# Performance work log

Measured on AMD Instinct MI355X. Metric: run time of the kernel, lower is better.

## Reference

```python
import jax, jax.numpy as jnp
import numpy as np

B, N, C = 16, 1024, 768
H, HD = 9, 64  # num_active_heads, head_dim


def setup_inputs() -> dict:
    key = jax.random.key(0)
    ks = jax.random.split(key, 5)
    x = jax.random.normal(ks[0], (B, N, C), dtype=jnp.float32)
    qkv_w = jax.random.normal(ks[1], (3 * H * HD, C), dtype=jnp.float32) * (1.0 / np.sqrt(C))
    qkv_b = jax.random.normal(ks[2], (3 * H * HD,), dtype=jnp.float32) * 0.02
    proj_w = jax.random.normal(ks[3], (C, H * HD), dtype=jnp.float32) * (1.0 / np.sqrt(H * HD))
    proj_b = jax.random.normal(ks[4], (C,), dtype=jnp.float32) * 0.02
    return {"x": x, "qkv_w": qkv_w, "qkv_b": qkv_b, "proj_w": proj_w, "proj_b": proj_b}


def reference(x, qkv_w, qkv_b, proj_w, proj_b):
    b, n, c = x.shape
    # qkv projection: [B,N,3*H*HD] -> [3,B,H,N,HD]
    qkv = (x @ qkv_w.T + qkv_b).reshape(b, n, 3, H, HD).transpose(2, 0, 3, 1, 4)
    q, k, v = qkv[0], qkv[1], qkv[2]
    scale = HD ** -0.5
    attn = jnp.einsum('bhqd,bhkd->bhqk', q, k) * scale  # [B,H,N,N]
    attn = jax.nn.softmax(attn, axis=-1)
    out = jnp.einsum('bhqk,bhkd->bhqd', attn, v)  # [B,H,N,HD]
    out = out.transpose(0, 2, 1, 3).reshape(b, n, H * HD)
    return out @ proj_w.T + proj_b
```

## Files before the change

### kernel.cpp

```cpp
#include <hip/hip_runtime.h>


typedef _Float16 f16x8 __attribute__((ext_vector_type(8)));
typedef _Float16 f16x4 __attribute__((ext_vector_type(4)));
typedef __fp16   h16x2 __attribute__((ext_vector_type(2)));
typedef float    f32x4 __attribute__((ext_vector_type(4)));

#define MFMA16(a, b, c) __builtin_amdgcn_mfma_f32_16x16x32_f16(a, b, c, 0, 0, 0)

__device__ __forceinline__ void gld16(const _Float16* g, _Float16* l) {
  __builtin_amdgcn_global_load_lds((const __attribute__((address_space(1))) void*)g,
                                   (__attribute__((address_space(3))) void*)l, 16, 0, 0);
}

__global__ __launch_bounds__(256) void cvt_swz(const float* __restrict__ src,
                                               _Float16* __restrict__ dst,
                                               int rows_src, int cpr, int total) {
  const int g = blockIdx.x * 256 + threadIdx.x;
  if (g >= total) return;
  const int row = g / cpr;
  const int c = g - row * cpr;
  const int L = cpr * 8;
  const int pos = (c & ~7) | ((c ^ row) & 7);
  union { f16x8 v; h16x2 h[4]; } u;
  if (row < rows_src) {
    const float4 a = *(const float4*)(src + row * L + c * 8);
    const float4 b = *(const float4*)(src + row * L + c * 8 + 4);
    u.h[0] = __builtin_amdgcn_cvt_pkrtz(a.x, a.y);
    u.h[1] = __builtin_amdgcn_cvt_pkrtz(a.z, a.w);
    u.h[2] = __builtin_amdgcn_cvt_pkrtz(b.x, b.y);
    u.h[3] = __builtin_amdgcn_cvt_pkrtz(b.z, b.w);
  } else {
    u.v = (f16x8){};
  }
  *(f16x8*)(dst + row * L + pos * 8) = u.v;
}

__global__ __launch_bounds__(256, 4) void gemm1_qkv(const _Float16* __restrict__ A,
                                                    const _Float16* __restrict__ Bw,
                                                    const float* __restrict__ bias,
                                                    _Float16* __restrict__ Qo,
                                                    _Float16* __restrict__ Ko,
                                                    _Float16* __restrict__ Vt) {
  __shared__ __align__(16) _Float16 As[128 * 64];
  __shared__ __align__(16) _Float16 Bs[128 * 64];
  const int tid = threadIdx.x;
  const int wave = tid >> 6, lane = tid & 63;
  const int lo = lane & 15, hi = lane >> 4;
  const int wm = (wave >> 1) * 64, wn = (wave & 1) * 64;
  const int g = blockIdx.x;
  const int xcd = g & 7, i = g >> 3;
  const int mt = i / 14, ntl = i - mt * 14;
  const int m0 = (xcd * 16 + mt) * 128, n0 = ntl * 128;
  f32x4 acc[4][4] = {};
  for (int k0 = 0; k0 < 768; k0 += 64) {
    __syncthreads();
    #pragma unroll
    for (int j = 0; j < 4; ++j) {
      const int seg = wave * 4 + j;
      const int gr = seg * 8 + (lane >> 3), gc = (lane & 7) << 3;
      gld16(A + (m0 + gr) * 768 + k0 + gc, As + seg * 512);
      gld16(Bw + (n0 + gr) * 768 + k0 + gc, Bs + seg * 512);
    }
    __syncthreads();
    #pragma unroll
    for (int ks = 0; ks < 2; ++ks) {
      f16x8 af[4], bf[4];
      const int p = ((ks * 4 + hi) ^ (lo & 7)) << 3;
      #pragma unroll
      for (int t = 0; t < 4; ++t) {
        af[t] = *(const f16x8*)(As + (wm + t * 16 + lo) * 64 + p);
        bf[t] = *(const f16x8*)(Bs + (wn + t * 16 + lo) * 64 + p);
      }
      #pragma unroll
      for (int mt2 = 0; mt2 < 4; ++mt2)
        #pragma unroll
        for (int nt = 0; nt < 4; ++nt)
          acc[mt2][nt] = MFMA16(af[mt2], bf[nt], acc[mt2][nt]);
    }
  }
  const int b = m0 >> 10;
  const int nrbase = (m0 & 1023) + wm;
  #pragma unroll
  for (int nt = 0; nt < 4; ++nt) {
    const int n = n0 + wn + nt * 16 + lo;
    if (n < 1728) {
      const float bv = bias[n];
      const int t3 = n / 576;
      const int rem = n - t3 * 576;
      const int hh = rem >> 6, d = rem & 63;
      const int bh16 = (b * 9 + hh) << 16;
      if (t3 == 2) {
        _Float16* dv = Vt + bh16 + d * 1024;
        #pragma unroll
        for (int mt2 = 0; mt2 < 4; ++mt2) {
          const int nr = nrbase + mt2 * 16 + hi * 4;
          const int c = nr >> 3;
          const int pos = (c & ~7) | ((c ^ d) & 7);
          union { f16x4 v; h16x2 h[2]; } u;
          u.h[0] = __builtin_amdgcn_cvt_pkrtz(acc[mt2][nt][0] + bv, acc[mt2][nt][1] + bv);
          u.h[1] = __builtin_amdgcn_cvt_pkrtz(acc[mt2][nt][2] + bv, acc[mt2][nt][3] + bv);
          *(f16x4*)(dv + pos * 8 + (nr & 7)) = u.v;
        }
      } else if (t3 == 1) {
        _Float16* dk = Ko + bh16;
        const int ch = d >> 3, dl = d & 7;
        #pragma unroll
        for (int mt2 = 0; mt2 < 4; ++mt2) {
          const int nr = nrbase + mt2 * 16 + hi * 4;
          #pragma unroll
          for (int i2 = 0; i2 < 4; ++i2) {
            const int t = nr + i2;
            dk[t * 64 + ((ch ^ (t & 7)) << 3) + dl] = (_Float16)(acc[mt2][nt][i2] + bv);
          }
        }
      } else {
        _Float16* dq = Qo + bh16 + d;
        #pragma unroll
        for (int mt2 = 0; mt2 < 4; ++mt2) {
          const int nr = nrbase + mt2 * 16 + hi * 4;
          #pragma unroll
          for (int i2 = 0; i2 < 4; ++i2)
            dq[(nr + i2) * 64] = (_Float16)(acc[mt2][nt][i2] + bv);
        }
      }
    }
  }
}

__global__ __launch_bounds__(256, 4) void attn_fused(const _Float16* __restrict__ Qg,
                                                     const _Float16* __restrict__ Kg,
                                                     const _Float16* __restrict__ Vtg,
                                                     _Float16* __restrict__ Og) {
  __shared__ __align__(16) _Float16 Ks[2][64 * 64];
  __shared__ __align__(16) _Float16 Vts[2][64 * 64];
  __shared__ __align__(16) _Float16 Ps[4][16 * 64];
  const int tid = threadIdx.x;
  const int wave = tid >> 6, lane = tid & 63;
  const int lo = lane & 15, hi = lane >> 4;
  const int bid = blockIdx.x;
  const int xcd = bid & 7, idx = bid >> 3;
  const int bh = xcd * 18 + (idx >> 4);
  const int q0 = (idx & 15) << 6;
  const _Float16* Qp  = Qg + (bh << 16);
  const _Float16* Kp  = Kg + (bh << 16);
  const _Float16* Vtp = Vtg + (bh << 16);

  auto issue = [&](int t0, int nb) {
    #pragma unroll
    for (int j = 0; j < 2; ++j) {
      const int seg = wave * 2 + j;
      gld16(Kp + (t0 + seg * 8 + (lane >> 3)) * 64 + ((lane & 7) << 3), &Ks[nb][seg * 512]);
      gld16(Vtp + (seg * 8 + (lane >> 3)) * 1024 + t0 + ((lane & 7) << 3), &Vts[nb][seg * 512]);
    }
  };

  issue(0, 0);

  f16x8 qf[2];
  const _Float16* qrow = Qp + (q0 + wave * 16 + lo) * 64;
  qf[0] = *(const f16x8*)(qrow + hi * 8);
  qf[1] = *(const f16x8*)(qrow + (4 + hi) * 8);

  float m_run = -1e30f, l_run = 0.f;
  f32x4 accO[4] = {};
  const float cs = 0.125f * 1.44269504f;
  _Float16* Pw = Ps[wave];

  auto compute = [&](int cb) {
    const _Float16* Kc = Ks[cb];
    const _Float16* Vc = Vts[cb];
    f32x4 sacc[4] = {};
    #pragma unroll
    for (int tt = 0; tt < 4; ++tt)
      #pragma unroll
      for (int ks = 0; ks < 2; ++ks) {
        const f16x8 kf = *(const f16x8*)(Kc + (tt * 16 + lo) * 64 + (((ks * 4 + hi) ^ (lo & 7)) << 3));
        sacc[tt] = MFMA16(kf, qf[ks], sacc[tt]);
      }
    float rmax = -1e30f;
    #pragma unroll
    for (int tt = 0; tt < 4; ++tt)
      rmax = fmaxf(rmax, fmaxf(fmaxf(sacc[tt][0], sacc[tt][1]), fmaxf(sacc[tt][2], sacc[tt][3])));
    rmax = fmaxf(rmax, __shfl_xor(rmax, 16, 64));
    rmax = fmaxf(rmax, __shfl_xor(rmax, 32, 64));
    const float rs = rmax * cs;
    const bool nsk = !__all(rs <= m_run + 8.f);
    const float mnew = nsk ? fmaxf(m_run, rs) : m_run;
    const float alpha = nsk ? __builtin_amdgcn_exp2f(m_run - mnew) : 1.f;
    float rsum = 0.f;
    #pragma unroll
    for (int tt = 0; tt < 4; ++tt) {
      const float p0 = __builtin_amdgcn_exp2f(fmaf(sacc[tt][0], cs, -mnew));
      const float p1 = __builtin_amdgcn_exp2f(fmaf(sacc[tt][1], cs, -mnew));
      const float p2 = __builtin_amdgcn_exp2f(fmaf(sacc[tt][2], cs, -mnew));
      const float p3 = __builtin_amdgcn_exp2f(fmaf(sacc[tt][3], cs, -mnew));
      rsum += (p0 + p1) + (p2 + p3);
      union { f16x4 v; h16x2 h[2]; } u;
      u.h[0] = __builtin_amdgcn_cvt_pkrtz(p0, p1);
      u.h[1] = __builtin_amdgcn_cvt_pkrtz(p2, p3);
      const int c = 2 * tt + (hi >> 1);
      *(f16x4*)(Pw + lo * 64 + (((c ^ lo) & 7) << 3) + ((hi & 1) << 2)) = u.v;
    }
    rsum += __shfl_xor(rsum, 16, 64);
    rsum += __shfl_xor(rsum, 32, 64);
    l_run = l_run * alpha + rsum;
    m_run = mnew;
    if (nsk) {
      #pragma unroll
      for (int dt = 0; dt < 4; ++dt) accO[dt] *= alpha;
    }

    #pragma unroll
    for (int ks2 = 0; ks2 < 2; ++ks2) {
      const int c = 4 * ks2 + hi;
      const f16x8 pf = *(const f16x8*)(Pw + lo * 64 + (((c ^ lo) & 7) << 3));
      #pragma unroll
      for (int dt = 0; dt < 4; ++dt) {
        const int dd = dt * 16 + lo;
        const f16x8 vf = *(const f16x8*)(Vc + dd * 64 + (((c ^ dd) & 7) << 3));
        accO[dt] = MFMA16(vf, pf, accO[dt]);
      }
    }
  };

  auto step = [&](int tnext0, int cb, bool pre) {
    if (pre) {
      issue(tnext0, cb ^ 1);
      asm volatile("s_waitcnt vmcnt(4)" ::: "memory");
    } else {
      asm volatile("s_waitcnt vmcnt(0)" ::: "memory");
    }
    __builtin_amdgcn_sched_barrier(0);
    __builtin_amdgcn_s_barrier();
    compute(cb);
    __builtin_amdgcn_sched_barrier(0);
    __builtin_amdgcn_s_barrier();
  };

  #pragma unroll 1
  for (int it = 0; it < 7; ++it) {
    step((2 * it + 1) << 6, 0, true);
    step((2 * it + 2) << 6, 1, true);
  }
  step(15 << 6, 0, true);
  step(0, 1, false);

  const float inv = 1.f / l_run;
  const int b = bh / 9, hh = bh - b * 9;
  const int rq = (b << 10) + q0 + wave * 16 + lo;
  #pragma unroll
  for (int dt = 0; dt < 4; ++dt) {
    union { f16x4 v; h16x2 h[2]; } u;
    u.h[0] = __builtin_amdgcn_cvt_pkrtz(accO[dt][0] * inv, accO[dt][1] * inv);
    u.h[1] = __builtin_amdgcn_cvt_pkrtz(accO[dt][2] * inv, accO[dt][3] * inv);
    const int c = hh * 8 + dt * 2 + (hi >> 1);
    const int pos = (c & ~7) | ((c ^ rq) & 7);
    *(f16x4*)(Og + rq * 576 + pos * 8 + ((hi & 1) << 2)) = u.v;
  }
}

__global__ __launch_bounds__(256, 4) void gemm3_proj(const _Float16* __restrict__ A,
                                                     const _Float16* __restrict__ Bw,
                                                     const float* __restrict__ bias,
                                                     float* __restrict__ out) {
  __shared__ __align__(16) _Float16 As[128 * 64];
  __shared__ __align__(16) _Float16 Bs[128 * 64];
  const int tid = threadIdx.x;
  const int wave = tid >> 6, lane = tid & 63;
  const int lo = lane & 15, hi = lane >> 4;
  const int wm = (wave >> 1) * 64, wn = (wave & 1) * 64;
  const int g = blockIdx.x;
  const int xcd = g & 7, i = g >> 3;
  const int mt = i / 6, ntl = i - mt * 6;
  const int m0 = (xcd * 16 + mt) * 128, n0 = ntl * 128;
  f32x4 acc[4][4] = {};
  for (int k0 = 0; k0 < 576; k0 += 64) {
    __syncthreads();
    #pragma unroll
    for (int j = 0; j < 4; ++j) {
      const int seg = wave * 4 + j;
      const int gr = seg * 8 + (lane >> 3), gc = (lane & 7) << 3;
      gld16(A + (m0 + gr) * 576 + k0 + gc, As + seg * 512);
      gld16(Bw + (n0 + gr) * 576 + k0 + gc, Bs + seg * 512);
    }
    __syncthreads();
    #pragma unroll
    for (int ks = 0; ks < 2; ++ks) {
      f16x8 af[4], bf[4];
      const int p = ((ks * 4 + hi) ^ (lo & 7)) << 3;
      #pragma unroll
      for (int t = 0; t < 4; ++t) {
        af[t] = *(const f16x8*)(As + (wm + t * 16 + lo) * 64 + p);
        bf[t] = *(const f16x8*)(Bs + (wn + t * 16 + lo) * 64 + p);
      }
      #pragma unroll
      for (int mt2 = 0; mt2 < 4; ++mt2)
        #pragma unroll
        for (int nt = 0; nt < 4; ++nt)
          acc[mt2][nt] = MFMA16(af[mt2], bf[nt], acc[mt2][nt]);
    }
  }
  #pragma unroll
  for (int nt = 0; nt < 4; ++nt) {
    const int n = n0 + wn + nt * 16 + lo;
    const float bv = bias[n];
    #pragma unroll
    for (int mt2 = 0; mt2 < 4; ++mt2) {
      const int mrow = m0 + wm + mt2 * 16 + hi * 4;
      #pragma unroll
      for (int i2 = 0; i2 < 4; ++i2)
        out[(mrow + i2) * 768 + n] = acc[mt2][nt][i2] + bv;
    }
  }
}

extern "C" void kernel_launch(void* const* d_in, const int* in_sizes, int n_in,
                              void* d_out, int out_size, void* d_ws, size_t ws_size,
                              hipStream_t stream) {
  const float* x      = (const float*)d_in[0];
  const float* qkv_w  = (const float*)d_in[1];
  const float* qkv_b  = (const float*)d_in[2];
  const float* proj_w = (const float*)d_in[3];
  const float* proj_b = (const float*)d_in[4];
  float* out = (float*)d_out;

  char* ws = (char*)d_ws;
  _Float16* x16 = (_Float16*)(ws + 0);
  _Float16* w1p = (_Float16*)(ws + 25165824);
  _Float16* w2h = (_Float16*)(ws + 27918336);
  _Float16* Qh  = (_Float16*)(ws + 28803072);
  _Float16* Kh  = (_Float16*)(ws + 47677440);
  _Float16* Vth = (_Float16*)(ws + 66551808);
  _Float16* Oh  = (_Float16*)(ws + 85426176);

  cvt_swz<<<6144, 256, 0, stream>>>(x, x16, 16384, 96, 16384 * 96);
  cvt_swz<<<672, 256, 0, stream>>>(qkv_w, w1p, 1728, 96, 1792 * 96);
  cvt_swz<<<216, 256, 0, stream>>>(proj_w, w2h, 768, 72, 768 * 72);
  gemm1_qkv<<<1792, 256, 0, stream>>>(x16, w1p, qkv_b, Qh, Kh, Vth);
  attn_fused<<<2304, 256, 0, stream>>>(Qh, Kh, Vth, Oh);
  gemm3_proj<<<768, 256, 0, stream>>>(Oh, w2h, proj_b, out);
}
```

Before: 247.4 us.

## Single-buffer V tile in attention to raise occupancy, add MFMA priority hints

The attention kernel now keeps a single LDS buffer for the V tile instead of two. The next V tile is loaded only after the end-of-step barrier, while K stays double-buffered and is prefetched at the start of each step. This frees LDS so the launch bound can request 5 blocks per CU instead of 4. s_setprio is also raised around the MFMA sections. The cost is that each V load is exposed within a single step's QK and softmax phase rather than a full iteration, and the vmcnt accounting changes.

Measured after the change: 244.4 us. About the same (-1.2%).

```diff
diff --git a/kernel.cpp b/kernel.cpp
--- a/kernel.cpp
+++ b/kernel.cpp
@@ -128,12 +128,12 @@
   }
 }
 
-__global__ __launch_bounds__(256, 4) void attn_fused(const _Float16* __restrict__ Qg,
+__global__ __launch_bounds__(256, 5) void attn_fused(const _Float16* __restrict__ Qg,
                                                      const _Float16* __restrict__ Kg,
                                                      const _Float16* __restrict__ Vtg,
                                                      _Float16* __restrict__ Og) {
   __shared__ __align__(16) _Float16 Ks[2][64 * 64];
-  __shared__ __align__(16) _Float16 Vts[2][64 * 64];
+  __shared__ __align__(16) _Float16 Vts[64 * 64];
   __shared__ __align__(16) _Float16 Ps[4][16 * 64];
   const int tid = threadIdx.x;
   const int wave = tid >> 6, lane = tid & 63;
@@ -146,16 +146,23 @@
   const _Float16* Kp  = Kg + (bh << 16);
   const _Float16* Vtp = Vtg + (bh << 16);
 
-  auto issue = [&](int t0, int nb) {
+  auto issueK = [&](int t0, int nb) {
     #pragma unroll
     for (int j = 0; j < 2; ++j) {
       const int seg = wave * 2 + j;
       gld16(Kp + (t0 + seg * 8 + (lane >> 3)) * 64 + ((lane & 7) << 3), &Ks[nb][seg * 512]);
-      gld16(Vtp + (seg * 8 + (lane >> 3)) * 1024 + t0 + ((lane & 7) << 3), &Vts[nb][seg * 512]);
     }
   };
-
-  issue(0, 0);
+  auto issueV = [&](int t0) {
+    #pragma unroll
+    for (int j = 0; j < 2; ++j) {
+      const int seg = wave * 2 + j;
+      gld16(Vtp + (seg * 8 + (lane >> 3)) * 1024 + t0 + ((lane & 7) << 3), Vts + seg * 512);
+    }
+  };
+
+  issueK(0, 0);
+  issueV(0);
 
   f16x8 qf[2];
   const _Float16* qrow = Qp + (q0 + wave * 16 + lo) * 64;
@@ -169,8 +176,8 @@
 
   auto compute = [&](int cb) {
     const _Float16* Kc = Ks[cb];
-    const _Float16* Vc = Vts[cb];
     f32x4 sacc[4] = {};
+    __builtin_amdgcn_s_setprio(1);
     #pragma unroll
     for (int tt = 0; tt < 4; ++tt)
       #pragma unroll
@@ -178,6 +185,7 @@
         const f16x8 kf = *(const f16x8*)(Kc + (tt * 16 + lo) * 64 + (((ks * 4 + hi) ^ (lo & 7)) << 3));
         sacc[tt] = MFMA16(kf, qf[ks], sacc[tt]);
       }
+    __builtin_amdgcn_s_setprio(0);
     float rmax = -1e30f;
     #pragma unroll
     for (int tt = 0; tt < 4; ++tt)
@@ -211,6 +219,7 @@
       for (int dt = 0; dt < 4; ++dt) accO[dt] *= alpha;
     }
 
+    __builtin_amdgcn_s_setprio(1);
     #pragma unroll
     for (int ks2 = 0; ks2 < 2; ++ks2) {
       const int c = 4 * ks2 + hi;
@@ -218,16 +227,17 @@
       #pragma unroll
       for (int dt = 0; dt < 4; ++dt) {
         const int dd = dt * 16 + lo;
-        const f16x8 vf = *(const f16x8*)(Vc + dd * 64 + (((c ^ dd) & 7) << 3));
+        const f16x8 vf = *(const f16x8*)(Vts + dd * 64 + (((c ^ dd) & 7) << 3));
         accO[dt] = MFMA16(vf, pf, accO[dt]);
       }
     }
+    __builtin_amdgcn_s_setprio(0);
   };
 
-  auto step = [&](int tnext0, int cb, bool pre) {
-    if (pre) {
-      issue(tnext0, cb ^ 1);
-      asm volatile("s_waitcnt vmcnt(4)" ::: "memory");
+  auto step = [&](int tn0, int cb, bool preK, bool preV) {
+    if (preK) {
+      issueK(tn0, cb ^ 1);
+      asm volatile("s_waitcnt vmcnt(2)" ::: "memory");
     } else {
       asm volatile("s_waitcnt vmcnt(0)" ::: "memory");
     }
@@ -236,15 +246,16 @@
     compute(cb);
     __builtin_amdgcn_sched_barrier(0);
     __builtin_amdgcn_s_barrier();
+    if (preV) issueV(tn0);
   };
 
   #pragma unroll 1
   for (int it = 0; it < 7; ++it) {
-    step((2 * it + 1) << 6, 0, true);
-    step((2 * it + 2) << 6, 1, true);
-  }
-  step(15 << 6, 0, true);
-  step(0, 1, false);
+    step((2 * it + 1) << 6, 0, true, true);
+    step((2 * it + 2) << 6, 1, true, true);
+  }
+  step(15 << 6, 0, true, true);
+  step(0, 1, false, false);
 
   const float inv = 1.f / l_run;
   const int b = bh / 9, hh = bh - b * 9;
```
